# Kernel tuning notes

Hardware: AMD Instinct MI355X
Metric: run time of the kernel (lower is better)

The kernel has to match this reference:

```python
import jax, jax.numpy as jnp
import numpy as np

D_MODEL, N_LAYER, VOCAB = 1024, 4, 50280
D_INNER, D_STATE, D_CONV, DT_RANK = 2048, 16, 4, 64
B, L = 1, 1024
EPS = 1e-5


def _rmsnorm(x, w):
    var = jnp.mean(jnp.square(x), axis=-1, keepdims=True)
    return x * jax.lax.rsqrt(var + EPS) * w


def _selective_scan(u, dt, A, Bm, Cm, Dv):
    # u, dt: [b,l,d]; A: [d,n]; Bm, Cm: [b,l,n]; Dv: [d]
    dA = jnp.exp(dt[..., None] * A)                      # [b,l,d,n]
    dBu = dt[..., None] * Bm[:, :, None, :] * u[..., None]  # [b,l,d,n]

    def step(s, x):
        dA_t, dBu_t, C_t = x
        s = s * dA_t + dBu_t                             # [b,d,n]
        y = jnp.einsum('bdn,bn->bd', s, C_t)
        return s, y

    s0 = jnp.zeros((u.shape[0], u.shape[2], A.shape[1]), u.dtype)
    xs = (dA.transpose(1, 0, 2, 3), dBu.transpose(1, 0, 2, 3), Cm.transpose(1, 0, 2))
    _, ys = jax.lax.scan(step, s0, xs)                   # ys: [l,b,d]
    return ys.transpose(1, 0, 2) + u * Dv


def _mixer(x, in_w, cw, cb, xp_w, dt_w, dt_b, A_log, Dv, out_w):
    Lx = x.shape[1]
    xz = jnp.einsum('bld,ed->ble', x, in_w)              # [b,l,2*d_inner]
    xp, z = jnp.split(xz, 2, axis=-1)
    # causal depthwise conv1d, kernel size D_CONV
    xpad = jnp.pad(xp, ((0, 0), (D_CONV - 1, 0), (0, 0)))
    conv = cb + sum(xpad[:, k:k + Lx, :] * cw[:, k] for k in range(D_CONV))
    u = jax.nn.silu(conv)
    xdbl = jnp.einsum('bld,ed->ble', u, xp_w)            # [b,l,dt_rank+2n]
    dt_r = xdbl[..., :DT_RANK]
    Bm = xdbl[..., DT_RANK:DT_RANK + D_STATE]
    Cm = xdbl[..., DT_RANK + D_STATE:]
    dt = jax.nn.softplus(jnp.einsum('blr,dr->bld', dt_r, dt_w) + dt_b)
    A = -jnp.exp(A_log)
    y = _selective_scan(u, dt, A, Bm, Cm, Dv)
    y = y * jax.nn.silu(z)
    return jnp.einsum('bld,ed->ble', y, out_w)


def _forward(input_ids, embedding, norm_w, in_proj_w, conv_w, conv_b, x_proj_w,
             dt_proj_w, dt_proj_b, A_log, D, out_proj_w, norm_f_w):
    hidden = embedding[input_ids]                        # [b,l,d_model]
    residual = None
    for i in range(N_LAYER):
        residual = hidden if residual is None else hidden + residual
        x = _rmsnorm(residual, norm_w[i])
        hidden = _mixer(x, in_proj_w[i], conv_w[i], conv_b[i], x_proj_w[i],
                        dt_proj_w[i], dt_proj_b[i], A_log[i], D[i], out_proj_w[i])
    residual = hidden + residual
    hf = _rmsnorm(residual, norm_f_w)
    # lm_head weight is tied to embedding
    return jnp.einsum('bld,vd->blv', hf, embedding)


def setup_inputs() -> dict:
    key = jax.random.key(0)
    ks = jax.random.split(key, 8)
    s = 0.02
    return {
        'input_ids': jax.random.randint(ks[0], (B, L), 0, VOCAB),
        'embedding': jax.random.normal(ks[1], (VOCAB, D_MODEL), jnp.float32) * s,
        'norm_w': jnp.ones((N_LAYER, D_MODEL), jnp.float32),
        'in_proj_w': jax.random.normal(ks[2], (N_LAYER, 2 * D_INNER, D_MODEL), jnp.float32) * s,
        'conv_w': jax.random.normal(ks[3], (N_LAYER, D_INNER, D_CONV), jnp.float32) * s,
        'conv_b': jnp.zeros((N_LAYER, D_INNER), jnp.float32),
        'x_proj_w': jax.random.normal(ks[4], (N_LAYER, DT_RANK + 2 * D_STATE, D_INNER), jnp.float32) * s,
        'dt_proj_w': jax.random.normal(ks[5], (N_LAYER, D_INNER, DT_RANK), jnp.float32) * s,
        'dt_proj_b': jnp.full((N_LAYER, D_INNER), -4.6, jnp.float32),  # softplus ~= 0.01
        'A_log': jnp.tile(jnp.log(jnp.arange(1.0, D_STATE + 1.0, dtype=jnp.float32))[None, None, :],
                          (N_LAYER, D_INNER, 1)),
        'D': jnp.ones((N_LAYER, D_INNER), jnp.float32),
        'out_proj_w': jax.random.normal(ks[6], (N_LAYER, D_MODEL, D_INNER), jnp.float32) * s,
        'norm_f_w': jnp.ones((D_MODEL,), jnp.float32),
    }


def reference(input_ids, embedding, norm_w, in_proj_w, conv_w, conv_b, x_proj_w,
              dt_proj_w, dt_proj_b, A_log, D, out_proj_w, norm_f_w):
    return _forward(input_ids, embedding, norm_w, in_proj_w, conv_w, conv_b,
                    x_proj_w, dt_proj_w, dt_proj_b, A_log, D, out_proj_w, norm_f_w)
```

## Files before the change

### kernel.cpp

```cpp
#include <hip/hip_runtime.h>
#include <hip/hip_bf16.h>

#define D_MODEL 1024
#define N_LAYER 4
#define D_INNER 2048
#define D_STATE 16
#define D_CONV  4
#define DT_RANK 64
#define SEQ_L   1024
#define VOCAB   50280
#define VOCAB_PAD 50304
#define NCHUNK  32
#define CLEN    32

typedef __attribute__((ext_vector_type(8))) short short8;
typedef __attribute__((ext_vector_type(4))) float f32x4;

typedef __attribute__((address_space(1))) const unsigned GUint;
typedef __attribute__((address_space(3))) unsigned LUint;

__device__ __forceinline__ float silu_f(float x) {
    return x / (1.0f + __expf(-x));
}
__device__ __forceinline__ float softplus_f(float x) {
    return fmaxf(x, 0.0f) + log1pf(__expf(-fabsf(x)));
}
__device__ __forceinline__ ushort f2bf(float f) {
    union { float f; unsigned u; } uf; uf.f = f;
    unsigned r = uf.u + 0x7FFF + ((uf.u >> 16) & 1);
    return (ushort)(r >> 16);
}
__device__ __forceinline__ float bf2f(ushort u) {
    union { unsigned u; float f; } x; x.u = ((unsigned)u) << 16; return x.f;
}

__global__ void f32_to_bf16_kernel(const float* __restrict__ in,
                                   ushort* __restrict__ out, int n4) {
    int i = blockIdx.x * 256 + threadIdx.x;
    if (i >= n4) return;
    float4 v = *(const float4*)(in + (size_t)i * 4);
    ushort4 o;
    o.x = f2bf(v.x); o.y = f2bf(v.y); o.z = f2bf(v.z); o.w = f2bf(v.w);
    *(ushort4*)(out + (size_t)i * 4) = o;
}

__global__ void xpw_convert_kernel(const float* __restrict__ src,
                                   ushort* __restrict__ dst) {
    int q = blockIdx.x * 256 + threadIdx.x;
    int layer = q / (128 * 512);
    int rq    = q % (128 * 512);
    int row   = rq / 512;
    int cq    = rq % 512;
    ushort4 o;
    if (row < 96) {
        float4 v = *(const float4*)(src + ((size_t)layer * 96 + row) * 2048 + cq * 4);
        o.x = f2bf(v.x); o.y = f2bf(v.y); o.z = f2bf(v.z); o.w = f2bf(v.w);
    } else {
        o.x = o.y = o.z = o.w = 0;
    }
    *(ushort4*)(dst + (size_t)q * 4) = o;
}

__global__ void embed_kernel(const int* __restrict__ ids,
                             const float* __restrict__ emb,
                             float* __restrict__ hidden) {
    int l = blockIdx.x;
    int t = threadIdx.x;
    int id = ids[l];
    float4 v = *(const float4*)(emb + (size_t)id * D_MODEL + t * 4);
    *(float4*)(hidden + (size_t)l * D_MODEL + t * 4) = v;
}

__global__ void add_rmsnorm_kernel(float* __restrict__ res,
                                   const float* __restrict__ part,
                                   const float* __restrict__ w,
                                   ushort* __restrict__ xout,
                                   int add, int nparts) {
    int l = blockIdx.x;
    int t = threadIdx.x;
    size_t base = (size_t)l * D_MODEL + t * 4;
    float4 r;
    if (add) r = *(const float4*)(res + base);
    else     r = make_float4(0.f, 0.f, 0.f, 0.f);
    for (int s = 0; s < nparts; ++s) {
        float4 hv = *(const float4*)(part + (size_t)s * SEQ_L * D_MODEL + base);
        r.x += hv.x; r.y += hv.y; r.z += hv.z; r.w += hv.w;
    }
    *(float4*)(res + base) = r;
    float ss = r.x * r.x + r.y * r.y + r.z * r.z + r.w * r.w;
    #pragma unroll
    for (int off = 32; off > 0; off >>= 1) ss += __shfl_down(ss, off, 64);
    __shared__ float sred[4];
    if ((t & 63) == 0) sred[t >> 6] = ss;
    __syncthreads();
    float tot = sred[0] + sred[1] + sred[2] + sred[3];
    float scale = rsqrtf(tot * (1.0f / (float)D_MODEL) + 1e-5f);
    float4 wv = *(const float4*)(w + t * 4);
    ushort4 o;
    o.x = f2bf(r.x * scale * wv.x);
    o.y = f2bf(r.y * scale * wv.y);
    o.z = f2bf(r.z * scale * wv.z);
    o.w = f2bf(r.w * scale * wv.w);
    *(ushort4*)(xout + base) = o;
}

template<int SPLIT, int OUTB>
__global__ void gemm_bf16_gld_kernel(const ushort* __restrict__ A,
                                     const ushort* __restrict__ W,
                                     void* __restrict__ Cv,
                                     int N, int K, int lda, int ldc,
                                     int MB, int KS, int pstride) {
    __shared__ ushort As[2][128][32];
    __shared__ ushort Ws[2][128][32];
    const int t  = threadIdx.x;
    const int T  = gridDim.x >> 3;
    const int id = blockIdx.x;
    const int j  = (id & 7) * T + (id >> 3);
    const int ks  = j % KS;
    const int rem = j / KS;
    const int m0 = (rem % MB) * 128;
    const int n0 = (rem / MB) * 128;
    const int kchunk = K / KS;
    const int kbeg = ks * kchunk;
    const int kend = kbeg + kchunk;

    const int lane = t & 63;
    const int w    = t >> 6;
    const int srow = w * 16 + (lane >> 2);
    const int scol = (((lane & 3) ^ ((lane >> 3) & 3)) * 8);
    const ushort* Ag0 = A + (size_t)(m0 + srow) * lda + scol;
    const ushort* Ag1 = A + (size_t)(m0 + srow + 64) * lda + scol;
    const ushort* Wg0 = W + (size_t)(n0 + srow) * K + scol;
    const ushort* Wg1 = W + (size_t)(n0 + srow + 64) * K + scol;

    const int wm = (t >> 7) & 1;
    const int wn = (t >> 6) & 1;
    const int lr = lane & 15;
    const int lk = lane >> 4;
    const int swz = (lr >> 1) & 3;

    f32x4 acc[4][4] = {};

#define STAGE_GLD(buf, kk)                                                        \
    do {                                                                          \
        __builtin_amdgcn_global_load_lds((GUint*)(Ag0 + (kk)),                    \
            (LUint*)&As[buf][w * 16][0], 16, 0, 0);                               \
        __builtin_amdgcn_global_load_lds((GUint*)(Ag1 + (kk)),                    \
            (LUint*)&As[buf][64 + w * 16][0], 16, 0, 0);                          \
        __builtin_amdgcn_global_load_lds((GUint*)(Wg0 + (kk)),                    \
            (LUint*)&Ws[buf][w * 16][0], 16, 0, 0);                               \
        __builtin_amdgcn_global_load_lds((GUint*)(Wg1 + (kk)),                    \
            (LUint*)&Ws[buf][64 + w * 16][0], 16, 0, 0);                          \
    } while (0)

    STAGE_GLD(0, kbeg);
    int buf = 0;
    for (int k0 = kbeg;;) {
        __syncthreads();
        const bool more = (k0 + 32) < kend;
        if (more) STAGE_GLD(buf ^ 1, k0 + 32);

        short8 af[4], bfr[4];
        #pragma unroll
        for (int m = 0; m < 4; ++m)
            af[m] = *(const short8*)&As[buf][wm * 64 + m * 16 + lr][(lk ^ swz) * 8];
        #pragma unroll
        for (int n = 0; n < 4; ++n)
            bfr[n] = *(const short8*)&Ws[buf][wn * 64 + n * 16 + lr][(lk ^ swz) * 8];
        #pragma unroll
        for (int m = 0; m < 4; ++m)
            #pragma unroll
            for (int n = 0; n < 4; ++n)
                acc[m][n] = __builtin_amdgcn_mfma_f32_16x16x32_bf16(
                    af[m], bfr[n], acc[m][n], 0, 0, 0);

        if (!more) break;
        buf ^= 1;
        k0 += 32;
    }
#undef STAGE_GLD

    float*  Cf = SPLIT ? ((float*)Cv + (size_t)ks * pstride) : (float*)Cv;
    ushort* Cb = (ushort*)Cv;
    #pragma unroll
    for (int m = 0; m < 4; ++m) {
        const int row = m0 + wm * 64 + m * 16 + lk * 4;
        #pragma unroll
        for (int n = 0; n < 4; ++n) {
            const int col = n0 + wn * 64 + n * 16 + lr;
            if (col < N) {
                #pragma unroll
                for (int r = 0; r < 4; ++r) {
                    if (OUTB)
                        Cb[(size_t)(row + r) * ldc + col] = f2bf(acc[m][n][r]);
                    else
                        Cf[(size_t)(row + r) * ldc + col] = acc[m][n][r];
                }
            }
        }
    }
}

__global__ void xdbl_reduce_kernel(const float* __restrict__ part,
                                   float* __restrict__ out) {
    int i = blockIdx.x * 256 + threadIdx.x;
    float4 acc = make_float4(0.f, 0.f, 0.f, 0.f);
    #pragma unroll
    for (int s = 0; s < 16; ++s) {
        float4 v = *(const float4*)(part + (size_t)s * SEQ_L * 96 + (size_t)i * 4);
        acc.x += v.x; acc.y += v.y; acc.z += v.z; acc.w += v.w;
    }
    *(float4*)(out + (size_t)i * 4) = acc;
}

template<int EPI>
__global__ void gemm_tn_kernel(const float* __restrict__ A,
                               const float* __restrict__ W,
                               const float* __restrict__ bias,
                               float* __restrict__ C,
                               int M, int N, int K, int lda) {
    __shared__ float As[16][68];
    __shared__ float Ws[16][68];
    const int t  = threadIdx.x;
    const int m0 = blockIdx.y * 64;
    const int n0 = blockIdx.x * 64;
    const int lrow = t >> 2;
    const int lkq  = (t & 3) * 4;
    const int tx = t & 15;
    const int ty = t >> 4;

    const float* Arow = A + (size_t)(m0 + lrow) * lda;
    const int   wr    = n0 + lrow;
    const bool  wvalid = wr < N;
    const float* Wrow = W + (size_t)(wvalid ? wr : 0) * K;

    float acc[4][4] = {};
    for (int k0 = 0; k0 < K; k0 += 16) {
        float4 av = *(const float4*)(Arow + k0 + lkq);
        float4 wv = wvalid ? *(const float4*)(Wrow + k0 + lkq)
                           : make_float4(0.f, 0.f, 0.f, 0.f);
        As[lkq + 0][lrow] = av.x; As[lkq + 1][lrow] = av.y;
        As[lkq + 2][lrow] = av.z; As[lkq + 3][lrow] = av.w;
        Ws[lkq + 0][lrow] = wv.x; Ws[lkq + 1][lrow] = wv.y;
        Ws[lkq + 2][lrow] = wv.z; Ws[lkq + 3][lrow] = wv.w;
        __syncthreads();
        #pragma unroll
        for (int kk = 0; kk < 16; ++kk) {
            float4 a = *(const float4*)&As[kk][ty * 4];
            float4 b = *(const float4*)&Ws[kk][tx * 4];
            #pragma unroll
            for (int i = 0; i < 4; ++i) {
                float ai = (i == 0) ? a.x : (i == 1) ? a.y : (i == 2) ? a.z : a.w;
                acc[i][0] = fmaf(ai, b.x, acc[i][0]);
                acc[i][1] = fmaf(ai, b.y, acc[i][1]);
                acc[i][2] = fmaf(ai, b.z, acc[i][2]);
                acc[i][3] = fmaf(ai, b.w, acc[i][3]);
            }
        }
        __syncthreads();
    }

    const int colb = n0 + tx * 4;
    if (colb < N) {
        #pragma unroll
        for (int i = 0; i < 4; ++i) {
            int row = m0 + ty * 4 + i;
            float4 v = make_float4(acc[i][0], acc[i][1], acc[i][2], acc[i][3]);
            if (EPI == 1) {
                v.x = softplus_f(v.x + bias[colb + 0]);
                v.y = softplus_f(v.y + bias[colb + 1]);
                v.z = softplus_f(v.z + bias[colb + 2]);
                v.w = softplus_f(v.w + bias[colb + 3]);
            }
            *(float4*)(C + (size_t)row * N + colb) = v;
        }
    }
}

__global__ void conv_silu_kernel(const ushort* __restrict__ xz,
                                 const float* __restrict__ cw,
                                 const float* __restrict__ cb,
                                 ushort* __restrict__ u_b) {
    int idx = blockIdx.x * 256 + threadIdx.x;
    int l = idx >> 11;
    int c = idx & 2047;
    float acc = cb[c];
    float w0 = cw[c * 4 + 0], w1 = cw[c * 4 + 1], w2 = cw[c * 4 + 2], w3 = cw[c * 4 + 3];
    if (l >= 3) acc = fmaf(bf2f(xz[(size_t)(l - 3) * 4096 + c]), w0, acc);
    if (l >= 2) acc = fmaf(bf2f(xz[(size_t)(l - 2) * 4096 + c]), w1, acc);
    if (l >= 1) acc = fmaf(bf2f(xz[(size_t)(l - 1) * 4096 + c]), w2, acc);
    acc = fmaf(bf2f(xz[(size_t)l * 4096 + c]), w3, acc);
    u_b[idx] = f2bf(silu_f(acc));
}

__global__ void scan_a_kernel(const ushort* __restrict__ u_b,
                              const float* __restrict__ dt,
                              const float* __restrict__ xdbl,
                              const float* __restrict__ A_log,
                              ushort* __restrict__ yloc,
                              float* __restrict__ cumdt,
                              float* __restrict__ s_end) {
    const int idx = blockIdx.x * 256 + threadIdx.x;
    const int d = idx & 2047;
    const int c = idx >> 11;

    float Aa[16];
    #pragma unroll
    for (int q = 0; q < 4; ++q) {
        float4 al = *(const float4*)(A_log + (size_t)d * 16 + q * 4);
        Aa[q * 4 + 0] = -__expf(al.x);
        Aa[q * 4 + 1] = -__expf(al.y);
        Aa[q * 4 + 2] = -__expf(al.z);
        Aa[q * 4 + 3] = -__expf(al.w);
    }

    float s[16];
    #pragma unroll
    for (int n = 0; n < 16; ++n) s[n] = 0.0f;
    float cd = 0.0f;

    const int l0 = c * CLEN;
    for (int i = 0; i < CLEN; ++i) {
        const int l = l0 + i;
        const float dtl = dt[(size_t)l * 2048 + d];
        const float ul  = bf2f(u_b[(size_t)l * 2048 + d]);
        float Bn[16], Cn[16];
        const float* xbp = xdbl + (size_t)l * 96;
        *(float4*)&Bn[0]  = *(const float4*)(xbp + 64);
        *(float4*)&Bn[4]  = *(const float4*)(xbp + 68);
        *(float4*)&Bn[8]  = *(const float4*)(xbp + 72);
        *(float4*)&Bn[12] = *(const float4*)(xbp + 76);
        *(float4*)&Cn[0]  = *(const float4*)(xbp + 80);
        *(float4*)&Cn[4]  = *(const float4*)(xbp + 84);
        *(float4*)&Cn[8]  = *(const float4*)(xbp + 88);
        *(float4*)&Cn[12] = *(const float4*)(xbp + 92);
        cd += dtl;
        const float dtu = dtl * ul;
        float y = 0.0f;
        #pragma unroll
        for (int n = 0; n < 16; ++n) {
            float dA = __expf(dtl * Aa[n]);
            s[n] = fmaf(s[n], dA, dtu * Bn[n]);
            y = fmaf(s[n], Cn[n], y);
        }
        yloc[(size_t)l * 4096 + d] = f2bf(y);
        cumdt[(size_t)l * 2048 + d] = cd;
    }
    float* se = s_end + ((size_t)d * NCHUNK + c) * 16;
    #pragma unroll
    for (int q = 0; q < 4; ++q)
        *(float4*)(se + q * 4) = make_float4(s[q * 4], s[q * 4 + 1], s[q * 4 + 2], s[q * 4 + 3]);
}

__global__ void scan_b_kernel(const float* __restrict__ s_end,
                              const float* __restrict__ cumdt,
                              const float* __restrict__ A_log,
                              float* __restrict__ s_in) {
    const int idx = blockIdx.x * 256 + threadIdx.x;
    const int d = idx >> 4;
    const int n = idx & 15;
    const float Aa = -__expf(A_log[(size_t)d * 16 + n]);
    float s = 0.0f;
    #pragma unroll
    for (int c = 0; c < NCHUNK; ++c) {
        s_in[((size_t)d * NCHUNK + c) * 16 + n] = s;
        const float tot = cumdt[(size_t)(c * CLEN + CLEN - 1) * 2048 + d];
        s = s_end[((size_t)d * NCHUNK + c) * 16 + n] + __expf(Aa * tot) * s;
    }
}

__global__ void scan_c_kernel(const ushort* __restrict__ u_b,
                              const float* __restrict__ xdbl,
                              const float* __restrict__ A_log,
                              const float* __restrict__ Dv,
                              const ushort* __restrict__ xz,
                              const float* __restrict__ cumdt,
                              const float* __restrict__ s_in,
                              ushort* __restrict__ yb) {
    const int idx = blockIdx.x * 256 + threadIdx.x;
    const int l = idx >> 11;
    const int d = idx & 2047;
    const int c = l >> 5;

    const float cd = cumdt[idx];
    const float ul = bf2f(u_b[idx]);
    const float yv = bf2f(xz[(size_t)l * 4096 + d]);
    const float zv = bf2f(xz[(size_t)l * 4096 + 2048 + d]);
    const float* Cp = xdbl + (size_t)l * 96 + 80;
    const float* si = s_in + ((size_t)d * NCHUNK + c) * 16;

    float corr = 0.0f;
    #pragma unroll
    for (int q = 0; q < 4; ++q) {
        float4 al = *(const float4*)(A_log + (size_t)d * 16 + q * 4);
        float4 cv = *(const float4*)(Cp + q * 4);
        float4 sv = *(const float4*)(si + q * 4);
        corr = fmaf(cv.x * __expf(-__expf(al.x) * cd), sv.x, corr);
        corr = fmaf(cv.y * __expf(-__expf(al.y) * cd), sv.y, corr);
        corr = fmaf(cv.z * __expf(-__expf(al.z) * cd), sv.z, corr);
        corr = fmaf(cv.w * __expf(-__expf(al.w) * cd), sv.w, corr);
    }
    const float y = (yv + corr + Dv[d] * ul) * silu_f(zv);
    yb[idx] = f2bf(y);
}

extern "C" void kernel_launch(void* const* d_in, const int* in_sizes, int n_in,
                              void* d_out, int out_size, void* d_ws, size_t ws_size,
                              hipStream_t stream) {
    const int*   ids        = (const int*)d_in[0];
    const float* emb        = (const float*)d_in[1];
    const float* norm_w     = (const float*)d_in[2];
    const float* in_proj_w  = (const float*)d_in[3];
    const float* conv_w     = (const float*)d_in[4];
    const float* conv_b     = (const float*)d_in[5];
    const float* x_proj_w   = (const float*)d_in[6];
    const float* dt_proj_w  = (const float*)d_in[7];
    const float* dt_proj_b  = (const float*)d_in[8];
    const float* A_log      = (const float*)d_in[9];
    const float* Dv         = (const float*)d_in[10];
    const float* out_proj_w = (const float*)d_in[11];
    const float* norm_f_w   = (const float*)d_in[12];
    float* out = (float*)d_out;

    char* p = (char*)d_ws;
    ushort* emb_b  = (ushort*)p; p += (size_t)VOCAB_PAD * D_MODEL * 2;
    ushort* inw_b  = (ushort*)p; p += (size_t)N_LAYER * 4096 * 1024 * 2;
    ushort* outw_b = (ushort*)p; p += (size_t)N_LAYER * 1024 * 2048 * 2;
    ushort* xpw_b  = (ushort*)p; p += (size_t)N_LAYER * 128 * 2048 * 2;
    float* residual = (float*)p; p += (size_t)SEQ_L * D_MODEL * 4;
    float* hpart    = (float*)p; p += (size_t)4 * SEQ_L * D_MODEL * 4;
    float* xdpart   = (float*)p; p += (size_t)16 * SEQ_L * 96 * 4;
    float* xdbl     = (float*)p; p += (size_t)SEQ_L * 96 * 4;
    ushort* xb      = (ushort*)p; p += (size_t)SEQ_L * D_MODEL * 2;
    ushort* xzb     = (ushort*)p; p += (size_t)SEQ_L * 4096 * 2;
    ushort* u_b     = (ushort*)p; p += (size_t)SEQ_L * 2048 * 2;
    float* dtb      = (float*)p; p += (size_t)SEQ_L * 2048 * 4;
    ushort* yb      = (ushort*)p; p += (size_t)SEQ_L * 2048 * 2;
    float* cumdt    = (float*)p; p += (size_t)SEQ_L * 2048 * 4;
    float* s_end    = (float*)p; p += (size_t)D_INNER * NCHUNK * 16 * 4;
    float* s_in     = (float*)p; p += (size_t)D_INNER * NCHUNK * 16 * 4;

    dim3 blk(256);

    f32_to_bf16_kernel<<<dim3(VOCAB * D_MODEL / 4 / 256), blk, 0, stream>>>(
        emb, emb_b, VOCAB * D_MODEL / 4);
    f32_to_bf16_kernel<<<dim3(N_LAYER * 4096 * 1024 / 4 / 256), blk, 0, stream>>>(
        in_proj_w, inw_b, N_LAYER * 4096 * 1024 / 4);
    f32_to_bf16_kernel<<<dim3(N_LAYER * 1024 * 2048 / 4 / 256), blk, 0, stream>>>(
        out_proj_w, outw_b, N_LAYER * 1024 * 2048 / 4);
    xpw_convert_kernel<<<dim3(N_LAYER * 128 * 2048 / 4 / 256), blk, 0, stream>>>(
        x_proj_w, xpw_b);

    embed_kernel<<<dim3(SEQ_L), blk, 0, stream>>>(ids, emb, hpart);

    for (int i = 0; i < N_LAYER; ++i) {
        add_rmsnorm_kernel<<<dim3(SEQ_L), blk, 0, stream>>>(
            residual, hpart, norm_w + (size_t)i * D_MODEL, xb,
            i == 0 ? 0 : 1, i == 0 ? 1 : 4);

        gemm_bf16_gld_kernel<0, 1><<<dim3(256), blk, 0, stream>>>(
            xb, inw_b + (size_t)i * 4096 * 1024, xzb, 4096, 1024, 1024, 4096, 8, 1, 0);

        conv_silu_kernel<<<dim3(SEQ_L * D_INNER / 256), blk, 0, stream>>>(
            xzb, conv_w + (size_t)i * D_INNER * D_CONV, conv_b + (size_t)i * D_INNER,
            u_b);

        gemm_bf16_gld_kernel<1, 0><<<dim3(128), blk, 0, stream>>>(
            u_b, xpw_b + (size_t)i * 128 * 2048, xdpart, 96, 2048, 2048, 96,
            8, 16, SEQ_L * 96);
        xdbl_reduce_kernel<<<dim3(SEQ_L * 96 / 4 / 256), blk, 0, stream>>>(
            xdpart, xdbl);

        gemm_tn_kernel<1><<<dim3(D_INNER / 64, SEQ_L / 64), blk, 0, stream>>>(
            xdbl, dt_proj_w + (size_t)i * D_INNER * DT_RANK,
            dt_proj_b + (size_t)i * D_INNER, dtb,
            SEQ_L, D_INNER, DT_RANK, 96);

        scan_a_kernel<<<dim3(D_INNER * NCHUNK / 256), blk, 0, stream>>>(
            u_b, dtb, xdbl, A_log + (size_t)i * D_INNER * D_STATE, xzb, cumdt, s_end);
        scan_b_kernel<<<dim3(D_INNER * 16 / 256), blk, 0, stream>>>(
            s_end, cumdt, A_log + (size_t)i * D_INNER * D_STATE, s_in);
        scan_c_kernel<<<dim3(SEQ_L * D_INNER / 256), blk, 0, stream>>>(
            u_b, xdbl, A_log + (size_t)i * D_INNER * D_STATE,
            Dv + (size_t)i * D_INNER, xzb, cumdt, s_in, yb);

        gemm_bf16_gld_kernel<1, 0><<<dim3(256), blk, 0, stream>>>(
            yb, outw_b + (size_t)i * 1024 * 2048, hpart, 1024, 2048, 2048, 1024,
            8, 4, SEQ_L * D_MODEL);
    }

    add_rmsnorm_kernel<<<dim3(SEQ_L), blk, 0, stream>>>(
        residual, hpart, norm_f_w, xb, 1, 4);

    gemm_bf16_gld_kernel<0, 0><<<dim3(3144), blk, 0, stream>>>(
        xb, emb_b, out, VOCAB, 1024, 1024, VOCAB, 8, 1, 0);
}
```

Baseline: 795.4 us.

## Split-K in_proj GEMM, vectorize conv, merge weight conversion kernels

The in_proj GEMM now runs with a split-K of 2, doubling its block count. Each half writes a bf16 partial into a doubled xz buffer, and the conv and scan_c consumers add the two halves. The causal conv+SiLU kernel processes 8 channels per thread with 16-byte loads. The four fp32-to-bf16 weight conversion launches are merged into one kernel to cut launch overhead. Storing partials in bf16 adds some rounding error and extra memory traffic for the second partition.

```diff
diff --git a/kernel.cpp b/kernel.cpp
--- a/kernel.cpp
+++ b/kernel.cpp
@@ -34,31 +34,48 @@
     union { unsigned u; float f; } x; x.u = ((unsigned)u) << 16; return x.f;
 }
 
-__global__ void f32_to_bf16_kernel(const float* __restrict__ in,
-                                   ushort* __restrict__ out, int n4) {
+#define QC_EMB  12871680
+#define QC_IN    4194304
+#define QC_OUT   2097152
+#define QC_XPW    262144
+__global__ void convert_all_kernel(const float* __restrict__ emb,
+                                   const float* __restrict__ inw,
+                                   const float* __restrict__ outw,
+                                   const float* __restrict__ xpw,
+                                   ushort* __restrict__ emb_b,
+                                   ushort* __restrict__ inw_b,
+                                   ushort* __restrict__ outw_b,
+                                   ushort* __restrict__ xpw_b) {
     int i = blockIdx.x * 256 + threadIdx.x;
-    if (i >= n4) return;
-    float4 v = *(const float4*)(in + (size_t)i * 4);
+    const float* src;
+    ushort* dst;
+    if (i < QC_EMB) {
+        src = emb + (size_t)i * 4; dst = emb_b + (size_t)i * 4;
+    } else if ((i -= QC_EMB) < QC_IN) {
+        src = inw + (size_t)i * 4; dst = inw_b + (size_t)i * 4;
+    } else if ((i -= QC_IN) < QC_OUT) {
+        src = outw + (size_t)i * 4; dst = outw_b + (size_t)i * 4;
+    } else if ((i -= QC_OUT) < QC_XPW) {
+        int layer = i / (128 * 512);
+        int rq    = i % (128 * 512);
+        int row   = rq / 512;
+        int cq    = rq % 512;
+        ushort4 o;
+        if (row < 96) {
+            float4 v = *(const float4*)(xpw + ((size_t)layer * 96 + row) * 2048 + cq * 4);
+            o.x = f2bf(v.x); o.y = f2bf(v.y); o.z = f2bf(v.z); o.w = f2bf(v.w);
+        } else {
+            o.x = o.y = o.z = o.w = 0;
+        }
+        *(ushort4*)(xpw_b + (size_t)i * 4) = o;
+        return;
+    } else {
+        return;
+    }
+    float4 v = *(const float4*)src;
     ushort4 o;
     o.x = f2bf(v.x); o.y = f2bf(v.y); o.z = f2bf(v.z); o.w = f2bf(v.w);
-    *(ushort4*)(out + (size_t)i * 4) = o;
-}
-
-__global__ void xpw_convert_kernel(const float* __restrict__ src,
-                                   ushort* __restrict__ dst) {
-    int q = blockIdx.x * 256 + threadIdx.x;
-    int layer = q / (128 * 512);
-    int rq    = q % (128 * 512);
-    int row   = rq / 512;
-    int cq    = rq % 512;
-    ushort4 o;
-    if (row < 96) {
-        float4 v = *(const float4*)(src + ((size_t)layer * 96 + row) * 2048 + cq * 4);
-        o.x = f2bf(v.x); o.y = f2bf(v.y); o.z = f2bf(v.z); o.w = f2bf(v.w);
-    } else {
-        o.x = o.y = o.z = o.w = 0;
-    }
-    *(ushort4*)(dst + (size_t)q * 4) = o;
+    *(ushort4*)dst = o;
 }
 
 __global__ void embed_kernel(const int* __restrict__ ids,
@@ -180,8 +197,9 @@
     }
 #undef STAGE_GLD
 
-    float*  Cf = SPLIT ? ((float*)Cv + (size_t)ks * pstride) : (float*)Cv;
-    ushort* Cb = (ushort*)Cv;
+    const size_t poff = SPLIT ? (size_t)ks * pstride : 0;
+    float*  Cf = (float*)Cv + poff;
+    ushort* Cb = (ushort*)Cv + poff;
     #pragma unroll
     for (int m = 0; m < 4; ++m) {
         const int row = m0 + wm * 64 + m * 16 + lk * 4;
@@ -281,16 +299,30 @@
                                  const float* __restrict__ cw,
                                  const float* __restrict__ cb,
                                  ushort* __restrict__ u_b) {
-    int idx = blockIdx.x * 256 + threadIdx.x;
-    int l = idx >> 11;
-    int c = idx & 2047;
-    float acc = cb[c];
-    float w0 = cw[c * 4 + 0], w1 = cw[c * 4 + 1], w2 = cw[c * 4 + 2], w3 = cw[c * 4 + 3];
-    if (l >= 3) acc = fmaf(bf2f(xz[(size_t)(l - 3) * 4096 + c]), w0, acc);
-    if (l >= 2) acc = fmaf(bf2f(xz[(size_t)(l - 2) * 4096 + c]), w1, acc);
-    if (l >= 1) acc = fmaf(bf2f(xz[(size_t)(l - 1) * 4096 + c]), w2, acc);
-    acc = fmaf(bf2f(xz[(size_t)l * 4096 + c]), w3, acc);
-    u_b[idx] = f2bf(silu_f(acc));
+    int idx8 = blockIdx.x * 256 + threadIdx.x;
+    int l  = idx8 >> 8;
+    int c0 = (idx8 & 255) * 8;
+
+    float acc[8];
+    #pragma unroll
+    for (int e = 0; e < 8; ++e) acc[e] = cb[c0 + e];
+
+    #pragma unroll
+    for (int k = 0; k < 4; ++k) {
+        int ls = l - (3 - k);
+        if (ls < 0) continue;
+        short8 p0 = *(const short8*)(xz + (size_t)ls * 4096 + c0);
+        short8 p1 = *(const short8*)(xz + (size_t)SEQ_L * 4096 + (size_t)ls * 4096 + c0);
+        #pragma unroll
+        for (int e = 0; e < 8; ++e) {
+            float xv = bf2f((ushort)p0[e]) + bf2f((ushort)p1[e]);
+            acc[e] = fmaf(xv, cw[(c0 + e) * 4 + k], acc[e]);
+        }
+    }
+    short8 o;
+    #pragma unroll
+    for (int e = 0; e < 8; ++e) o[e] = (short)f2bf(silu_f(acc[e]));
+    *(short8*)(u_b + (size_t)l * 2048 + c0) = o;
 }
 
 __global__ void scan_a_kernel(const ushort* __restrict__ u_b,
@@ -385,7 +417,8 @@
     const float cd = cumdt[idx];
     const float ul = bf2f(u_b[idx]);
     const float yv = bf2f(xz[(size_t)l * 4096 + d]);
-    const float zv = bf2f(xz[(size_t)l * 4096 + 2048 + d]);
+    const float zv = bf2f(xz[(size_t)l * 4096 + 2048 + d])
+                   + bf2f(xz[(size_t)SEQ_L * 4096 + (size_t)l * 4096 + 2048 + d]);
     const float* Cp = xdbl + (size_t)l * 96 + 80;
     const float* si = s_in + ((size_t)d * NCHUNK + c) * 16;
 
@@ -432,7 +465,7 @@
     float* xdpart   = (float*)p; p += (size_t)16 * SEQ_L * 96 * 4;
     float* xdbl     = (float*)p; p += (size_t)SEQ_L * 96 * 4;
     ushort* xb      = (ushort*)p; p += (size_t)SEQ_L * D_MODEL * 2;
-    ushort* xzb     = (ushort*)p; p += (size_t)SEQ_L * 4096 * 2;
+    ushort* xzb     = (ushort*)p; p += (size_t)2 * SEQ_L * 4096 * 2;
     ushort* u_b     = (ushort*)p; p += (size_t)SEQ_L * 2048 * 2;
     float* dtb      = (float*)p; p += (size_t)SEQ_L * 2048 * 4;
     ushort* yb      = (ushort*)p; p += (size_t)SEQ_L * 2048 * 2;
@@ -442,14 +475,9 @@
 
     dim3 blk(256);
 
-    f32_to_bf16_kernel<<<dim3(VOCAB * D_MODEL / 4 / 256), blk, 0, stream>>>(
-        emb, emb_b, VOCAB * D_MODEL / 4);
-    f32_to_bf16_kernel<<<dim3(N_LAYER * 4096 * 1024 / 4 / 256), blk, 0, stream>>>(
-        in_proj_w, inw_b, N_LAYER * 4096 * 1024 / 4);
-    f32_to_bf16_kernel<<<dim3(N_LAYER * 1024 * 2048 / 4 / 256), blk, 0, stream>>>(
-        out_proj_w, outw_b, N_LAYER * 1024 * 2048 / 4);
-    xpw_convert_kernel<<<dim3(N_LAYER * 128 * 2048 / 4 / 256), blk, 0, stream>>>(
-        x_proj_w, xpw_b);
+    const int total_quads = QC_EMB + QC_IN + QC_OUT + QC_XPW;
+    convert_all_kernel<<<dim3((total_quads + 255) / 256), blk, 0, stream>>>(
+        emb, in_proj_w, out_proj_w, x_proj_w, emb_b, inw_b, outw_b, xpw_b);
 
     embed_kernel<<<dim3(SEQ_L), blk, 0, stream>>>(ids, emb, hpart);
 
@@ -458,10 +486,11 @@
             residual, hpart, norm_w + (size_t)i * D_MODEL, xb,
             i == 0 ? 0 : 1, i == 0 ? 1 : 4);
 
-        gemm_bf16_gld_kernel<0, 1><<<dim3(256), blk, 0, stream>>>(
-            xb, inw_b + (size_t)i * 4096 * 1024, xzb, 4096, 1024, 1024, 4096, 8, 1, 0);
-
-        conv_silu_kernel<<<dim3(SEQ_L * D_INNER / 256), blk, 0, stream>>>(
+        gemm_bf16_gld_kernel<1, 1><<<dim3(512), blk, 0, stream>>>(
+            xb, inw_b + (size_t)i * 4096 * 1024, xzb, 4096, 1024, 1024, 4096,
+            8, 2, SEQ_L * 4096);
+
+        conv_silu_kernel<<<dim3(SEQ_L * D_INNER / 8 / 256), blk, 0, stream>>>(
             xzb, conv_w + (size_t)i * D_INNER * D_CONV, conv_b + (size_t)i * D_INNER,
             u_b);
 
```

Result: slower. 814.8 us (+2.4%).
